# Optimization experiments

Measured on AMD Instinct MI355X. Metric: run time of the kernel, lower is better.

Reference implementation:

```python
import jax, jax.numpy as jnp
import numpy as np

GAMMA_MIN = 1e-4
BIG = 1e9  # stands in for +inf; exp(-BIG/gamma) == 0 exactly in fp32, avoids inf-inf NaNs
M, N, D = 4096, 4096, 512


def setup_inputs() -> dict:
    key = jax.random.key(0)
    k1, k2 = jax.random.split(key)
    x = jax.random.normal(k1, (M, D), dtype=jnp.float32)
    y = jax.random.normal(k2, (N, D), dtype=jnp.float32)
    gamma = jnp.asarray(1.0, dtype=jnp.float32)
    return {"x": x, "y": y, "gamma": gamma}


def _softmin(stacked, gamma):
    # softmin over axis 0: -gamma * logsumexp(-v / gamma)
    return -gamma * jax.nn.logsumexp(-stacked / gamma, axis=0)


def _forward_dp(cost, gamma):
    # Anti-diagonal wavefront. diag_d[i] = R[i, d - i] with R (m+1, n+1) DP, R[0,0]=0.
    m, n = cost.shape
    idx = jnp.arange(m + 1)
    diag0 = jnp.full((m + 1,), BIG, cost.dtype).at[0].set(0.0)  # d = 0
    diag1 = jnp.full((m + 1,), BIG, cost.dtype)                 # d = 1 (boundary = inf)

    def step(carry, d):
        prev2, prev1 = carry  # diag_{d-2}, diag_{d-1}
        j = d - idx
        valid = (idx >= 1) & (j >= 1) & (j <= n)
        c = cost[jnp.clip(idx - 1, 0, m - 1), jnp.clip(j - 1, 0, n - 1)]
        p2 = jnp.roll(prev2, 1).at[0].set(BIG)  # R[i-1, j-1]
        p1 = jnp.roll(prev1, 1).at[0].set(BIG)  # R[i-1, j]
        new = jnp.where(valid, c + _softmin(jnp.stack([p2, p1, prev1]), gamma), BIG)
        return (prev1, new), new

    _, diags = jax.lax.scan(step, (diag0, diag1), jnp.arange(2, m + n + 1))
    ii = jnp.arange(1, m + 1)[:, None]
    jj = jnp.arange(1, n + 1)[None, :]
    return diags[ii + jj - 2, ii]  # (m, n): dp_f at cell (i, j)


def _backward_dp(cost, gamma):
    # Reverse DP: E[m,n] = 0; E[i,j] = softmin over reachable successors + cost.
    m, n = cost.shape
    idx = jnp.arange(m + 1)
    diag_top = jnp.full((m + 1,), BIG, cost.dtype)               # d = m+n+1
    diag_mn = jnp.full((m + 1,), BIG, cost.dtype).at[m].set(0.0)  # d = m+n

    def cost_at(i0, j0):
        return cost[jnp.clip(i0, 0, m - 1), jnp.clip(j0, 0, n - 1)]

    def step(carry, d):
        nxt1, nxt2 = carry  # diag_{d+1}, diag_{d+2}
        j = d - idx
        valid = (idx >= 1) & (j >= 1) & (j <= n)
        n1 = jnp.roll(nxt1, -1).at[m].set(BIG)  # E[i+1, j]
        n2 = jnp.roll(nxt2, -1).at[m].set(BIG)  # E[i+1, j+1]
        ok1 = valid & (idx <= m - 1) & (j <= n - 1)
        ok2 = valid & (idx <= m - 1)
        ok3 = valid & (j <= n - 1)
        c1 = jnp.where(ok1, n2 + cost_at(idx, j), BIG)        # diag move
        c2 = jnp.where(ok2, n1 + cost_at(idx, j - 1), BIG)    # down move
        c3 = jnp.where(ok3, nxt1 + cost_at(idx - 1, j), BIG)  # right move
        new = jnp.where(valid, _softmin(jnp.stack([c1, c2, c3]), gamma), BIG)
        new = jnp.where((idx == m) & (j == n), 0.0, new)  # (m,n) stays 0
        return (new, nxt1), new

    _, diags = jax.lax.scan(step, (diag_mn, diag_top), jnp.arange(m + n - 1, 1, -1))
    diags_all = jnp.concatenate([diag_mn[None, :], diags], axis=0)  # row k holds d = m+n-k
    ii = jnp.arange(1, m + 1)[:, None]
    jj = jnp.arange(1, n + 1)[None, :]
    return diags_all[m + n - ii - jj, ii]  # (m, n)


def reference(x, y, gamma):
    g = jnp.maximum(jnp.abs(gamma), GAMMA_MIN)
    xn = x / jnp.maximum(jnp.linalg.norm(x, axis=-1, keepdims=True), 1e-12)
    yn = y / jnp.maximum(jnp.linalg.norm(y, axis=-1, keepdims=True), 1e-12)
    cost = 1.0 - xn @ yn.T  # (M, N) cosine distance
    dp_f = _forward_dp(cost, g)
    distance = dp_f[-1, -1]
    dp_b = _backward_dp(cost, g)
    log_p = jnp.minimum(-(dp_f + cost + dp_b - distance) / g, 0.0)
    alignment = jnp.exp(log_p)
    total = jnp.maximum(alignment.sum(), 1e-8)
    alignment = alignment / total * min(cost.shape)
    return alignment, distance
```

## Files before the change

### kernel.cpp

```cpp
#include <hip/hip_runtime.h>
#include <stdint.h>

#define MDIM 4096
#define NDIM 4096
#define DDIM 512
#define BIGV 1e9f
#define GAMMA_MIN 1e-4f

#define CH 32
#define NSTEPS (NDIM + 63)
#define NCHUNK ((NSTEPS + CH - 1) / CH)
#define CLO 2
#define CHI 127
#define WPB 4
#define NBR 16
#define NDPB (2 * NBR)
#define NHEAT 224

#define LOG2E_F 1.4426950408889634f
#define LN2_F   0.69314718055994531f
#define TAGBASE 0x5A5A0000u

__device__ __forceinline__ float f4c(const float4 v, int j) {
  switch (j & 3) { case 0: return v.x; case 1: return v.y; case 2: return v.z; default: return v.w; }
}
__device__ __forceinline__ float4 ld4u(const float* p) { return *(const float4*)p; }
typedef float f4a __attribute__((ext_vector_type(4), aligned(4)));
__device__ __forceinline__ void st4u(float* p, float a, float b, float c, float d) {
  f4a v = {a, b, c, d};
  *(f4a*)p = v;
}
__device__ __forceinline__ float wshr1o(float old, float x) {
  int r = __builtin_amdgcn_update_dpp(__builtin_bit_cast(int, old),
                                      __builtin_bit_cast(int, x), 0x138, 0xF, 0xF, false);
  return __builtin_bit_cast(float, r);
}
__device__ __forceinline__ uint64_t haloLoad1(const uint64_t* hbase, int col0, int lane) {
  int idx = col0 + (lane & 15);
  if (idx > NDIM - 1) idx = NDIM - 1;
  return __hip_atomic_load(hbase + idx, __ATOMIC_RELAXED, __HIP_MEMORY_SCOPE_AGENT);
}
__device__ __forceinline__ uint64_t haloSpin(const uint64_t* hbase, int col0, int lane,
                                             uint64_t cur) {
  int idx = col0 + (lane & 15);
  if (idx > NDIM - 1) idx = NDIM - 1;
  const uint32_t etag = TAGBASE | (uint32_t)idx;
  while (__ballot((uint32_t)(cur >> 32) == etag) != ~0ull) {
    __builtin_amdgcn_s_sleep(1);
    cur = __hip_atomic_load(hbase + idx, __ATOMIC_RELAXED, __HIP_MEMORY_SCOPE_AGENT);
  }
  return cur;
}
__device__ __forceinline__ void haloUnpack2(uint64_t w0, uint64_t w1, float* hA) {
  const int lo0 = (int)(uint32_t)(w0 & 0xFFFFFFFFull);
  const int lo1 = (int)(uint32_t)(w1 & 0xFFFFFFFFull);
#pragma unroll
  for (int s = 0; s < 16; ++s) {
    hA[s]      = __builtin_bit_cast(float, __builtin_amdgcn_readlane(lo0, s));
    hA[16 + s] = __builtin_bit_cast(float, __builtin_amdgcn_readlane(lo1, s));
  }
}
__device__ __forceinline__ void haloStore(uint64_t* hbase, int col, float v) {
  const uint64_t u = ((uint64_t)(TAGBASE | (uint32_t)col) << 32) |
                     (uint64_t)__builtin_bit_cast(uint32_t, v);
  __hip_atomic_store(hbase + col, u, __ATOMIC_RELAXED, __HIP_MEMORY_SCOPE_AGENT);
}
__device__ __forceinline__ int ldsFlagLoad(const int* p) {
  return __hip_atomic_load(p, __ATOMIC_RELAXED, __HIP_MEMORY_SCOPE_WORKGROUP);
}
__device__ __forceinline__ void ldsFlagStore(int* p, int v) {
  __hip_atomic_store(p, v, __ATOMIC_RELAXED, __HIP_MEMORY_SCOPE_WORKGROUP);
}

__global__ void init_small(double* __restrict__ sum_p, float* __restrict__ dist_p,
                           int* __restrict__ done_p) {
  if (threadIdx.x == 0) *sum_p = 0.0;
  if (threadIdx.x == 1) *dist_p = 0.0f;
  if (threadIdx.x == 2) *done_p = 0;
}

__global__ __launch_bounds__(128) void norm_rows(const float* __restrict__ x,
                                                 const float* __restrict__ y,
                                                 float* __restrict__ xn,
                                                 float* __restrict__ yn) {
  const int row = blockIdx.x;
  const float* src = (row < MDIM) ? (x + (size_t)row * DDIM) : (y + (size_t)(row - MDIM) * DDIM);
  float*       dst = (row < MDIM) ? (xn + (size_t)row * DDIM) : (yn + (size_t)(row - MDIM) * DDIM);
  float4 v = ((const float4*)src)[threadIdx.x];
  float ss = v.x * v.x + v.y * v.y + v.z * v.z + v.w * v.w;
#pragma unroll
  for (int off = 32; off > 0; off >>= 1) ss += __shfl_down(ss, off);
  __shared__ float acc[2];
  if ((threadIdx.x & 63) == 0) acc[threadIdx.x >> 6] = ss;
  __syncthreads();
  const float total = acc[0] + acc[1];
  const float inv = 1.0f / fmaxf(sqrtf(total), 1e-12f);
  v.x *= inv; v.y *= inv; v.z *= inv; v.w *= inv;
  ((float4*)dst)[threadIdx.x] = v;
}

#define GT 128
__global__ __launch_bounds__(256) void gemm_cost(const float* __restrict__ xn,
                                                 const float* __restrict__ yn,
                                                 float* __restrict__ cost) {
  __shared__ float As[16][GT + 4];
  __shared__ float Bs[16][GT + 4];
  const int t  = threadIdx.x;
  const int bx = blockIdx.x & 31;
  const int by = blockIdx.x >> 5;
  const int tx = t & 15, ty = t >> 4;
  const int lrow = t >> 1;
  const int lk   = (t & 1) * 8;
  const float* arow = xn + (size_t)(by * GT + lrow) * DDIM + lk;
  const float* brow = yn + (size_t)(bx * GT + lrow) * DDIM + lk;

  float acc[8][8];
#pragma unroll
  for (int i = 0; i < 8; ++i)
#pragma unroll
    for (int j = 0; j < 8; ++j) acc[i][j] = 0.0f;

  for (int kt = 0; kt < DDIM; kt += 16) {
    const float4 a0 = *(const float4*)(arow + kt);
    const float4 a1 = *(const float4*)(arow + kt + 4);
    const float4 b0 = *(const float4*)(brow + kt);
    const float4 b1 = *(const float4*)(brow + kt + 4);
    __syncthreads();
    As[lk + 0][lrow] = a0.x; As[lk + 1][lrow] = a0.y; As[lk + 2][lrow] = a0.z; As[lk + 3][lrow] = a0.w;
    As[lk + 4][lrow] = a1.x; As[lk + 5][lrow] = a1.y; As[lk + 6][lrow] = a1.z; As[lk + 7][lrow] = a1.w;
    Bs[lk + 0][lrow] = b0.x; Bs[lk + 1][lrow] = b0.y; Bs[lk + 2][lrow] = b0.z; Bs[lk + 3][lrow] = b0.w;
    Bs[lk + 4][lrow] = b1.x; Bs[lk + 5][lrow] = b1.y; Bs[lk + 6][lrow] = b1.z; Bs[lk + 7][lrow] = b1.w;
    __syncthreads();
#pragma unroll
    for (int k = 0; k < 16; ++k) {
      const float4 av0 = *(const float4*)&As[k][ty * 8];
      const float4 av1 = *(const float4*)&As[k][ty * 8 + 4];
      const float4 bv0 = *(const float4*)&Bs[k][tx * 8];
      const float4 bv1 = *(const float4*)&Bs[k][tx * 8 + 4];
      const float av[8] = {av0.x, av0.y, av0.z, av0.w, av1.x, av1.y, av1.z, av1.w};
      const float bv[8] = {bv0.x, bv0.y, bv0.z, bv0.w, bv1.x, bv1.y, bv1.z, bv1.w};
#pragma unroll
      for (int i = 0; i < 8; ++i)
#pragma unroll
        for (int j = 0; j < 8; ++j) acc[i][j] = fmaf(av[i], bv[j], acc[i][j]);
    }
  }
#pragma unroll
  for (int i = 0; i < 8; ++i) {
    const size_t row = (size_t)(by * GT + ty * 8 + i);
    float* o = cost + row * NDIM + bx * GT + tx * 8;
    const float4 o0 = make_float4(1.0f - acc[i][0], 1.0f - acc[i][1], 1.0f - acc[i][2], 1.0f - acc[i][3]);
    const float4 o1 = make_float4(1.0f - acc[i][4], 1.0f - acc[i][5], 1.0f - acc[i][6], 1.0f - acc[i][7]);
    *(float4*)o = o0;
    *(float4*)(o + 4) = o1;
  }
}

template <int DIR>
__device__ void run_band(const float* __restrict__ cost, float* __restrict__ dpOut,
                         uint64_t* __restrict__ halo, float* dist_out, float g,
                         int br, int w, int lane,
                         float* lhaloR, float* lhaloW, int* flagR, int* flagW) {
  const float k1 = LOG2E_F / g;
  const float k2 = g * LN2_F;
  const int b = br * WPB + w;
  const int r = b * 64 + lane;
  const float* crow = DIR ? (cost + (size_t)(MDIM - 1 - r) * NDIM + (NDIM - 1))
                          : (cost + (size_t)r * NDIM);
  float* myrow = dpOut + (size_t)r * NDIM;
  const bool top   = (b == 0);
  const bool ldsR  = (w > 0);
  const bool globR = (!top && !ldsR);
  const bool ldsW  = (w < WPB - 1);
  const bool globW = (!ldsW && br < NBR - 1);
  const uint64_t* ghR = halo + (size_t)(DIR * NBR + (br > 0 ? br - 1 : 0)) * NDIM;
  uint64_t*       ghW = halo + (size_t)(DIR * NBR + br) * NDIM;

  float v_prev = BIGV;
  float w2 = (top && lane == 0) ? 0.0f : BIGV;
  float vk  = v_prev * k1;
  float w2k = w2 * k1;
  float P_l = 0.0f, P_d = 0.0f;
  double Btot = 0.0;
  const float beta = exp2f(k1);

  float4 cc[8], cn1[8], cn2[8];
#pragma unroll
  for (int q = 0; q < 8; ++q) {
    const int cb0 = 0 * CH - lane, cb1 = 1 * CH - lane, cb2 = 2 * CH - lane;
    cc[q]  = DIR ? ld4u(crow - cb0 - 4 * q - 3) : ld4u(crow + cb0 + 4 * q);
    cn1[q] = DIR ? ld4u(crow - cb1 - 4 * q - 3) : ld4u(crow + cb1 + 4 * q);
    cn2[q] = DIR ? ld4u(crow - cb2 - 4 * q - 3) : ld4u(crow + cb2 + 4 * q);
  }

  float hA[CH];
  uint64_t hB0 = 0, hB1 = 0, hC0 = 0, hC1 = 0;
  if (globR) {
    uint64_t h0 = haloLoad1(ghR, 0, lane);
    h0 = haloSpin(ghR, 0, lane, h0);
    uint64_t h1 = haloLoad1(ghR, 16, lane);
    h1 = haloSpin(ghR, 16, lane, h1);
    haloUnpack2(h0, h1, hA);
    hB0 = haloLoad1(ghR, 1 * CH, lane);
    hB1 = haloLoad1(ghR, 1 * CH + 16, lane);
    hC0 = haloLoad1(ghR, 2 * CH, lane);
    hC1 = haloLoad1(ghR, 2 * CH + 16, lane);
  } else if (ldsR) {
    while (ldsFlagLoad(flagR) < 3) __builtin_amdgcn_s_sleep(1);
    asm volatile("" ::: "memory");
    const float4* lp = (const float4*)&lhaloR[0];
#pragma unroll
    for (int q = 0; q < 8; ++q) {
      const float4 hv = lp[q];
      hA[4 * q] = hv.x; hA[4 * q + 1] = hv.y; hA[4 * q + 2] = hv.z; hA[4 * q + 3] = hv.w;
    }
  }

  for (int c = 0; c < NCHUNK; ++c) {
    float buf[CH];
    const int t0 = c * CH;
    const int base = t0 - lane;
    if (c >= CLO && c <= CHI) {
      const double Tc0d = (double)(b * 64 + t0);
      if (c == CLO) {
        Btot = (double)v_prev - (Tc0d - 1.0);
        P_l  = 1.0f;
        P_d  = exp2f((v_prev - 1.0f - w2) * k1);
      } else {
        const int mb = __builtin_bit_cast(int, P_l);
        int E = ((mb >> 23) & 0xFF) - 127;
        E = E < -120 ? -120 : (E > 120 ? 120 : E);
        const float rho = __builtin_bit_cast(float, (127 - E) << 23);
        P_l *= rho; P_d *= rho;
        Btot -= (double)k2 * (double)E;
      }
      const double BtU = __shfl_up(Btot, 1);
      float fup = exp2f((float)(Btot - BtU) * k1);
      const float vbf = (float)(Tc0d + Btot);
      const double Bt0 = __shfl(Btot, 0);
      const float hcf = (float)(Tc0d - 1.0 + Bt0);
      int Ecum = 0, E0cum = 0;
#pragma unroll
      for (int qs = 0; qs < 8; ++qs) {
        if (qs) {
          const int mb2 = __builtin_bit_cast(int, P_l);
          int E = ((mb2 >> 23) & 0xFF) - 127;
          E = E < -120 ? -120 : (E > 120 ? 120 : E);
          const float rho = __builtin_bit_cast(float, (127 - E) << 23);
          int dE = __shfl_up(E, 1) - E;
          dE = dE < -120 ? -120 : (dE > 120 ? 120 : dE);
          const float fsc = __builtin_bit_cast(float, (127 + dE) << 23);
          const int E0 = __shfl(E, 0);
          P_l *= rho; P_d *= rho; fup *= fsc;
          Ecum += E; E0cum += E0;
        }
        const float Ecf = (float)Ecum;
        const float E0f = (float)E0cum;
#pragma unroll
        for (int si = 0; si < 4; ++si) {
          const int s = qs * 4 + si;
          const float targ = hcf + (float)s - hA[s];
          const float hps = top ? 0.0f : exp2f(fmaf(targ, k1, -E0f));
          const float Pu = wshr1o(hps, P_l) * fup;
          float S = Pu + P_l;
          S = fmaf(beta, P_d, S);
          const float cval = DIR ? f4c(cc[s >> 2], 3 - (s & 3)) : f4c(cc[s >> 2], s);
          const float Kv = exp2f(fmaf(-cval, k1, k1));
          const float P = Kv * S;
          buf[s] = fminf(fmaxf(fmaf(-k2, log2f(P) + Ecf, vbf + (float)s), -BIGV), BIGV);
          P_d = Pu; P_l = P;
        }
      }
      Btot -= (double)k2 * (double)Ecum;
    } else {
      if (c == CHI + 1) {
        const double TcBd = (double)(b * 64 + t0);
        v_prev = fminf(fmaf(-k2, log2f(P_l), (float)(TcBd - 1.0 + Btot)), BIGV);
        w2     = fminf(fmaf(-k2, log2f(P_d), (float)(TcBd - 2.0 + Btot)), BIGV);
        vk = v_prev * k1; w2k = w2 * k1;
      }
#pragma unroll
      for (int s = 0; s < CH; ++s) {
        const float hold = top ? BIGV : hA[s];
        const float w1 = wshr1o(hold, v_prev);
        const float w1k = w1 * k1;
        const float m = fminf(fminf(w2, w1), v_prev);
        const float e = exp2f(fmaf(m, k1, -w2k)) + exp2f(fmaf(m, k1, -w1k)) +
                        exp2f(fmaf(m, k1, -vk));
        const float cval = DIR ? f4c(cc[s >> 2], 3 - (s & 3)) : f4c(cc[s >> 2], s);
        const float v = fmaf(-k2, log2f(e), m + cval);
        buf[s] = v;
        const bool act = (base + s >= 0) && (base + s < NDIM);
        v_prev = act ? v : v_prev;
        vk     = act ? v * k1 : vk;
        w2 = w1; w2k = w1k;
      }
    }

    if (globR && c + 1 <= NDIM / CH) {
      hB0 = haloSpin(ghR, CH * (c + 1), lane, hB0);
      hB1 = haloSpin(ghR, CH * (c + 1) + 16, lane, hB1);
      haloUnpack2(hB0, hB1, hA);
      hB0 = hC0; hB1 = hC1;
      hC0 = haloLoad1(ghR, CH * (c + 3), lane);
      hC1 = haloLoad1(ghR, CH * (c + 3) + 16, lane);
    } else if (ldsR && c + 1 <= CHI) {
      int need = c + 4;
      if (need > NCHUNK) need = NCHUNK;
      while (ldsFlagLoad(flagR) < need) __builtin_amdgcn_s_sleep(1);
      asm volatile("" ::: "memory");
      const float4* lp = (const float4*)&lhaloR[CH * (c + 1)];
#pragma unroll
      for (int q = 0; q < 8; ++q) {
        const float4 hv = lp[q];
        hA[4 * q] = hv.x; hA[4 * q + 1] = hv.y; hA[4 * q + 2] = hv.z; hA[4 * q + 3] = hv.w;
      }
    }

#pragma unroll
    for (int q = 0; q < 8; ++q) { cc[q] = cn1[q]; cn1[q] = cn2[q]; }
    {
      const int cb = (c + 3) * CH - lane;
#pragma unroll
      for (int q = 0; q < 8; ++q)
        cn2[q] = DIR ? ld4u(crow - cb - 4 * q - 3) : ld4u(crow + cb + 4 * q);
    }

    if (c >= CLO && c <= CHI) {
#pragma unroll
      for (int q = 0; q < 8; ++q)
        st4u(myrow + base + 4 * q, buf[4 * q], buf[4 * q + 1], buf[4 * q + 2], buf[4 * q + 3]);
    } else {
#pragma unroll
      for (int s = 0; s < CH; ++s) {
        const int col = base + s;
        if (col >= 0 && col < NDIM) myrow[col] = buf[s];
      }
    }
    if (ldsW) {
      if (lane == 63) {
        if (c >= CLO && c <= CHI) {
#pragma unroll
          for (int s = 0; s < CH; ++s) lhaloW[base + s] = buf[s];
        } else {
#pragma unroll
          for (int s = 0; s < CH; ++s) {
            const int col = base + s;
            if (col >= 0 && col < NDIM) lhaloW[col] = buf[s];
          }
        }
      }
      asm volatile("s_waitcnt lgkmcnt(0)" ::: "memory");
      if (lane == 63) ldsFlagStore(flagW, c + 1);
    } else if (globW && lane == 63) {
      if (c >= CLO && c <= CHI) {
#pragma unroll
        for (int s = 0; s < CH; ++s) haloStore(ghW, base + s, buf[s]);
      } else {
#pragma unroll
        for (int s = 0; s < CH; ++s) {
          const int col = base + s;
          if (col >= 0 && col < NDIM) haloStore(ghW, col, buf[s]);
        }
      }
    }
  }
  if (DIR == 0 && b == 63 && lane == 63) *dist_out = v_prev;
}

__global__ __launch_bounds__(256, 1) void dp_kernel(const float* __restrict__ cost,
                                                    float* __restrict__ dpF, float* __restrict__ dpG,
                                                    uint64_t* __restrict__ halo, float* dist_out,
                                                    const float* __restrict__ gamma_p,
                                                    int* __restrict__ done_p) {
  if (blockIdx.x >= NDPB) {
    float t0 = (float)threadIdx.x + 1.0f, t1 = t0 + 0.5f, t2 = t0 + 0.25f, t3 = t0 + 0.125f;
    int off = (int)(blockIdx.x * 1031 + threadIdx.x);
    while (__hip_atomic_load(done_p, __ATOMIC_RELAXED, __HIP_MEMORY_SCOPE_AGENT) < NDPB) {
#pragma unroll 8
      for (int i = 0; i < 256; ++i) {
        t0 = fmaf(t0, 1.0000001f, 0.03125f);
        t1 = fmaf(t1, 0.9999999f, 0.03125f);
        t2 = fmaf(t2, 1.0000002f, 0.03125f);
        t3 = fmaf(t3, 0.9999998f, 0.03125f);
      }
      off = (off + 4099) & (MDIM * NDIM - 1);
      t0 = fmaf(cost[off], 1e-30f, t0);
    }
    if (t0 + t1 + t2 + t3 == -1.0f && threadIdx.x == 12345) *done_p = 99;
    return;
  }
  __shared__ float lh[WPB - 1][NDIM];
  __shared__ int   lf[WPB - 1];
  const int w = threadIdx.x >> 6, lane = threadIdx.x & 63;
  if (threadIdx.x < WPB - 1) lf[threadIdx.x] = 0;
  __syncthreads();
  const int dir = blockIdx.x >> 4;
  const int br  = blockIdx.x & 15;
  const float g = fmaxf(fabsf(gamma_p[0]), GAMMA_MIN);
  float* lhR = (w > 0) ? lh[w - 1] : nullptr;
  float* lhW = (w < WPB - 1) ? lh[w] : nullptr;
  int* fR = (w > 0) ? &lf[w - 1] : nullptr;
  int* fW = (w < WPB - 1) ? &lf[w] : nullptr;
  if (dir == 0) run_band<0>(cost, dpF, halo, dist_out, g, br, w, lane, lhR, lhW, fR, fW);
  else          run_band<1>(cost, dpG, halo, dist_out, g, br, w, lane, lhR, lhW, fR, fW);
  __syncthreads();
  if (threadIdx.x == 0)
    __hip_atomic_fetch_add(done_p, 1, __ATOMIC_RELAXED, __HIP_MEMORY_SCOPE_AGENT);
}

__global__ __launch_bounds__(256) void pass1(float* __restrict__ out, const float* __restrict__ dpG,
                                             const float* __restrict__ dist_p,
                                             const float* __restrict__ gamma_p,
                                             double* __restrict__ sum_p) {
  const size_t idx4 = (size_t)blockIdx.x * 256 + threadIdx.x;
  const size_t base = idx4 * 4;
  const float g = fmaxf(fabsf(gamma_p[0]), GAMMA_MIN);
  const float invg = 1.0f / g;
  const float dist = *dist_p;
  const float4 f = ((const float4*)out)[idx4];
  const float4 grev = ((const float4*)dpG)[(16777212u - base) >> 2];
  const float x0 = fminf((dist - f.x - grev.w) * invg, 0.0f);
  const float x1 = fminf((dist - f.y - grev.z) * invg, 0.0f);
  const float x2 = fminf((dist - f.z - grev.y) * invg, 0.0f);
  const float x3 = fminf((dist - f.w - grev.x) * invg, 0.0f);
  const float a0 = exp2f(x0 * LOG2E_F), a1 = exp2f(x1 * LOG2E_F);
  const float a2 = exp2f(x2 * LOG2E_F), a3 = exp2f(x3 * LOG2E_F);
  ((float4*)out)[idx4] = make_float4(a0, a1, a2, a3);
  float s = a0 + a1 + a2 + a3;
#pragma unroll
  for (int off = 32; off > 0; off >>= 1) s += __shfl_down(s, off);
  __shared__ float wsum[4];
  if ((threadIdx.x & 63) == 0) wsum[threadIdx.x >> 6] = s;
  __syncthreads();
  if (threadIdx.x == 0) atomicAdd(sum_p, (double)(wsum[0] + wsum[1] + wsum[2] + wsum[3]));
}

__global__ __launch_bounds__(256) void pass2(float* __restrict__ out,
                                             const double* __restrict__ sum_p,
                                             const float* __restrict__ dist_p) {
  const size_t idx4 = (size_t)blockIdx.x * 256 + threadIdx.x;
  const float total = fmaxf((float)*sum_p, 1e-8f);
  const float scale = 4096.0f / total;
  float4 v = ((const float4*)out)[idx4];
  v.x *= scale; v.y *= scale; v.z *= scale; v.w *= scale;
  ((float4*)out)[idx4] = v;
  if (idx4 == 0) out[16777216] = *dist_p;
}

extern "C" void kernel_launch(void* const* d_in, const int* in_sizes, int n_in,
                              void* d_out, int out_size, void* d_ws, size_t ws_size,
                              hipStream_t stream) {
  const float* x = (const float*)d_in[0];
  const float* y = (const float*)d_in[1];
  const float* gamma_p = (const float*)d_in[2];
  float* out = (float*)d_out;

  uint8_t* w = (uint8_t*)d_ws;
  const size_t SZ_MAT = (size_t)MDIM * NDIM * sizeof(float);
  const size_t SZ_XN  = (size_t)MDIM * DDIM * sizeof(float);
  float* xn  = (float*)w;
  float* yn  = (float*)(w + SZ_XN);
  float* dpG = (float*)w;
  float* cost = (float*)(w + SZ_MAT + 512);
  uint8_t* small = w + SZ_MAT + 512 + SZ_MAT + 512;
  double* sum_p  = (double*)small;
  float*  dist_p = (float*)(small + 8);
  int*    done_p = (int*)(small + 16);
  uint64_t* halo = (uint64_t*)d_in[0];

  hipLaunchKernelGGL(init_small, dim3(1), dim3(64), 0, stream, sum_p, dist_p, done_p);
  hipLaunchKernelGGL(norm_rows, dim3(2 * MDIM), dim3(128), 0, stream, x, y, xn, yn);
  hipLaunchKernelGGL(gemm_cost, dim3((MDIM / GT) * (NDIM / GT)), dim3(256), 0, stream, xn, yn, cost);
  hipLaunchKernelGGL(dp_kernel, dim3(NDPB + NHEAT), dim3(64 * WPB), 0, stream,
                     cost, out, dpG, halo, dist_p, gamma_p, done_p);
  hipLaunchKernelGGL(pass1, dim3(MDIM * NDIM / 1024), dim3(256), 0, stream, out, dpG, dist_p, gamma_p, sum_p);
  hipLaunchKernelGGL(pass2, dim3(MDIM * NDIM / 1024), dim3(256), 0, stream, out, sum_p, dist_p);
}
```

Before: 2.057 ms.

## Run one 64-row DP band per single-wave workgroup, chaining bands through global halo

Each 64-row band now runs in its own single-wave workgroup, so the intra-block LDS halo handoff and its flag polling are removed. All 64 bands per direction hand boundary values through tagged global atomics instead. A large dummy LDS array pads each block, likely to force one DP band per CU, and the heater blocks now spin more lightly with sleeps. This spreads the DP waves over more CUs but puts every band-to-band handoff on the slower global-memory path.

```diff
diff --git a/kernel.cpp b/kernel.cpp
--- a/kernel.cpp
+++ b/kernel.cpp
@@ -12,10 +12,9 @@
 #define NCHUNK ((NSTEPS + CH - 1) / CH)
 #define CLO 2
 #define CHI 127
-#define WPB 4
-#define NBR 16
-#define NDPB (2 * NBR)
-#define NHEAT 224
+#define NBANDS 64
+#define NDPB (2 * NBANDS)
+#define NHEAT 128
 
 #define LOG2E_F 1.4426950408889634f
 #define LN2_F   0.69314718055994531f
@@ -64,12 +63,6 @@
   const uint64_t u = ((uint64_t)(TAGBASE | (uint32_t)col) << 32) |
                      (uint64_t)__builtin_bit_cast(uint32_t, v);
   __hip_atomic_store(hbase + col, u, __ATOMIC_RELAXED, __HIP_MEMORY_SCOPE_AGENT);
-}
-__device__ __forceinline__ int ldsFlagLoad(const int* p) {
-  return __hip_atomic_load(p, __ATOMIC_RELAXED, __HIP_MEMORY_SCOPE_WORKGROUP);
-}
-__device__ __forceinline__ void ldsFlagStore(int* p, int v) {
-  __hip_atomic_store(p, v, __ATOMIC_RELAXED, __HIP_MEMORY_SCOPE_WORKGROUP);
 }
 
 __global__ void init_small(double* __restrict__ sum_p, float* __restrict__ dist_p,
@@ -159,22 +152,18 @@
 template <int DIR>
 __device__ void run_band(const float* __restrict__ cost, float* __restrict__ dpOut,
                          uint64_t* __restrict__ halo, float* dist_out, float g,
-                         int br, int w, int lane,
-                         float* lhaloR, float* lhaloW, int* flagR, int* flagW) {
+                         int b, int lane) {
   const float k1 = LOG2E_F / g;
   const float k2 = g * LN2_F;
-  const int b = br * WPB + w;
   const int r = b * 64 + lane;
   const float* crow = DIR ? (cost + (size_t)(MDIM - 1 - r) * NDIM + (NDIM - 1))
                           : (cost + (size_t)r * NDIM);
   float* myrow = dpOut + (size_t)r * NDIM;
   const bool top   = (b == 0);
-  const bool ldsR  = (w > 0);
-  const bool globR = (!top && !ldsR);
-  const bool ldsW  = (w < WPB - 1);
-  const bool globW = (!ldsW && br < NBR - 1);
-  const uint64_t* ghR = halo + (size_t)(DIR * NBR + (br > 0 ? br - 1 : 0)) * NDIM;
-  uint64_t*       ghW = halo + (size_t)(DIR * NBR + br) * NDIM;
+  const bool globR = !top;
+  const bool globW = (b < NBANDS - 1);
+  const uint64_t* ghR = halo + (size_t)(DIR * NBANDS + (b > 0 ? b - 1 : 0)) * NDIM;
+  uint64_t*       ghW = halo + (size_t)(DIR * NBANDS + b) * NDIM;
 
   float v_prev = BIGV;
   float w2 = (top && lane == 0) ? 0.0f : BIGV;
@@ -205,15 +194,6 @@
     hB1 = haloLoad1(ghR, 1 * CH + 16, lane);
     hC0 = haloLoad1(ghR, 2 * CH, lane);
     hC1 = haloLoad1(ghR, 2 * CH + 16, lane);
-  } else if (ldsR) {
-    while (ldsFlagLoad(flagR) < 3) __builtin_amdgcn_s_sleep(1);
-    asm volatile("" ::: "memory");
-    const float4* lp = (const float4*)&lhaloR[0];
-#pragma unroll
-    for (int q = 0; q < 8; ++q) {
-      const float4 hv = lp[q];
-      hA[4 * q] = hv.x; hA[4 * q + 1] = hv.y; hA[4 * q + 2] = hv.z; hA[4 * q + 3] = hv.w;
-    }
   }
 
   for (int c = 0; c < NCHUNK; ++c) {
@@ -304,17 +284,6 @@
       hB0 = hC0; hB1 = hC1;
       hC0 = haloLoad1(ghR, CH * (c + 3), lane);
       hC1 = haloLoad1(ghR, CH * (c + 3) + 16, lane);
-    } else if (ldsR && c + 1 <= CHI) {
-      int need = c + 4;
-      if (need > NCHUNK) need = NCHUNK;
-      while (ldsFlagLoad(flagR) < need) __builtin_amdgcn_s_sleep(1);
-      asm volatile("" ::: "memory");
-      const float4* lp = (const float4*)&lhaloR[CH * (c + 1)];
-#pragma unroll
-      for (int q = 0; q < 8; ++q) {
-        const float4 hv = lp[q];
-        hA[4 * q] = hv.x; hA[4 * q + 1] = hv.y; hA[4 * q + 2] = hv.z; hA[4 * q + 3] = hv.w;
-      }
     }
 
 #pragma unroll
@@ -337,22 +306,7 @@
         if (col >= 0 && col < NDIM) myrow[col] = buf[s];
       }
     }
-    if (ldsW) {
-      if (lane == 63) {
-        if (c >= CLO && c <= CHI) {
-#pragma unroll
-          for (int s = 0; s < CH; ++s) lhaloW[base + s] = buf[s];
-        } else {
-#pragma unroll
-          for (int s = 0; s < CH; ++s) {
-            const int col = base + s;
-            if (col >= 0 && col < NDIM) lhaloW[col] = buf[s];
-          }
-        }
-      }
-      asm volatile("s_waitcnt lgkmcnt(0)" ::: "memory");
-      if (lane == 63) ldsFlagStore(flagW, c + 1);
-    } else if (globW && lane == 63) {
+    if (globW && lane == 63) {
       if (c >= CLO && c <= CHI) {
 #pragma unroll
         for (int s = 0; s < CH; ++s) haloStore(ghW, base + s, buf[s]);
@@ -365,46 +319,38 @@
       }
     }
   }
-  if (DIR == 0 && b == 63 && lane == 63) *dist_out = v_prev;
-}
-
-__global__ __launch_bounds__(256, 1) void dp_kernel(const float* __restrict__ cost,
-                                                    float* __restrict__ dpF, float* __restrict__ dpG,
-                                                    uint64_t* __restrict__ halo, float* dist_out,
-                                                    const float* __restrict__ gamma_p,
-                                                    int* __restrict__ done_p) {
+  if (DIR == 0 && b == NBANDS - 1 && lane == 63) *dist_out = v_prev;
+}
+
+__global__ __launch_bounds__(64, 1) void dp_kernel(const float* __restrict__ cost,
+                                                   float* __restrict__ dpF, float* __restrict__ dpG,
+                                                   uint64_t* __restrict__ halo, float* dist_out,
+                                                   const float* __restrict__ gamma_p,
+                                                   int* __restrict__ done_p) {
+  __shared__ float pad_lds[10240];
+  if (__builtin_bit_cast(int, gamma_p[0]) == 0x7F123456)
+    ((volatile float*)pad_lds)[threadIdx.x & 63] = 1.0f;
+
   if (blockIdx.x >= NDPB) {
-    float t0 = (float)threadIdx.x + 1.0f, t1 = t0 + 0.5f, t2 = t0 + 0.25f, t3 = t0 + 0.125f;
+    float t = (float)threadIdx.x + 1.0f;
     int off = (int)(blockIdx.x * 1031 + threadIdx.x);
     while (__hip_atomic_load(done_p, __ATOMIC_RELAXED, __HIP_MEMORY_SCOPE_AGENT) < NDPB) {
-#pragma unroll 8
-      for (int i = 0; i < 256; ++i) {
-        t0 = fmaf(t0, 1.0000001f, 0.03125f);
-        t1 = fmaf(t1, 0.9999999f, 0.03125f);
-        t2 = fmaf(t2, 1.0000002f, 0.03125f);
-        t3 = fmaf(t3, 0.9999998f, 0.03125f);
-      }
       off = (off + 4099) & (MDIM * NDIM - 1);
-      t0 = fmaf(cost[off], 1e-30f, t0);
-    }
-    if (t0 + t1 + t2 + t3 == -1.0f && threadIdx.x == 12345) *done_p = 99;
+      const float cv = cost[off];
+#pragma unroll
+      for (int i = 0; i < 24; ++i) t = fmaf(t, 1.0000001f, 0.03125f);
+      t = fmaf(cv, 1e-30f, t);
+      __builtin_amdgcn_s_sleep(8);
+    }
+    if (t == -1.0f && threadIdx.x == 12345) *done_p = 99;
     return;
   }
-  __shared__ float lh[WPB - 1][NDIM];
-  __shared__ int   lf[WPB - 1];
-  const int w = threadIdx.x >> 6, lane = threadIdx.x & 63;
-  if (threadIdx.x < WPB - 1) lf[threadIdx.x] = 0;
-  __syncthreads();
-  const int dir = blockIdx.x >> 4;
-  const int br  = blockIdx.x & 15;
+  const int lane = (int)(threadIdx.x & 63);
+  const int dir  = (int)(blockIdx.x >> 6);
+  const int b    = (int)(blockIdx.x & 63);
   const float g = fmaxf(fabsf(gamma_p[0]), GAMMA_MIN);
-  float* lhR = (w > 0) ? lh[w - 1] : nullptr;
-  float* lhW = (w < WPB - 1) ? lh[w] : nullptr;
-  int* fR = (w > 0) ? &lf[w - 1] : nullptr;
-  int* fW = (w < WPB - 1) ? &lf[w] : nullptr;
-  if (dir == 0) run_band<0>(cost, dpF, halo, dist_out, g, br, w, lane, lhR, lhW, fR, fW);
-  else          run_band<1>(cost, dpG, halo, dist_out, g, br, w, lane, lhR, lhW, fR, fW);
-  __syncthreads();
+  if (dir == 0) run_band<0>(cost, dpF, halo, dist_out, g, b, lane);
+  else          run_band<1>(cost, dpG, halo, dist_out, g, b, lane);
   if (threadIdx.x == 0)
     __hip_atomic_fetch_add(done_p, 1, __ATOMIC_RELAXED, __HIP_MEMORY_SCOPE_AGENT);
 }
@@ -472,7 +418,7 @@
   hipLaunchKernelGGL(init_small, dim3(1), dim3(64), 0, stream, sum_p, dist_p, done_p);
   hipLaunchKernelGGL(norm_rows, dim3(2 * MDIM), dim3(128), 0, stream, x, y, xn, yn);
   hipLaunchKernelGGL(gemm_cost, dim3((MDIM / GT) * (NDIM / GT)), dim3(256), 0, stream, xn, yn, cost);
-  hipLaunchKernelGGL(dp_kernel, dim3(NDPB + NHEAT), dim3(64 * WPB), 0, stream,
+  hipLaunchKernelGGL(dp_kernel, dim3(NDPB + NHEAT), dim3(64), 0, stream,
                      cost, out, dpG, halo, dist_p, gamma_p, done_p);
   hipLaunchKernelGGL(pass1, dim3(MDIM * NDIM / 1024), dim3(256), 0, stream, out, dpG, dist_p, gamma_p, sum_p);
   hipLaunchKernelGGL(pass2, dim3(MDIM * NDIM / 1024), dim3(256), 0, stream, out, sum_p, dist_p);
```

New measurement: 2.270 ms. 1.1x slower.
